# Optimization experiments

Measured on AMD Instinct MI355X. Metric: run time of the kernel, lower is better.

## Reference

```python
import jax, jax.numpy as jnp
import numpy as np

B, T, I, H = 4096, 512, 3, 64


def setup_inputs() -> dict:
    key = jax.random.key(0)
    ks = jax.random.split(key, 8)
    s = 1.0 / np.sqrt(H)  # PyTorch LSTM init scale
    x = jax.random.normal(ks[0], (B, T, I), dtype=jnp.float32)
    W_ih = jax.random.uniform(ks[1], (4 * H, I), minval=-s, maxval=s, dtype=jnp.float32)
    W_hh = jax.random.uniform(ks[2], (4 * H, H), minval=-s, maxval=s, dtype=jnp.float32)
    b_ih = jax.random.uniform(ks[3], (4 * H,), minval=-s, maxval=s, dtype=jnp.float32)
    b_hh = jax.random.uniform(ks[4], (4 * H,), minval=-s, maxval=s, dtype=jnp.float32)
    W_dec = jax.random.uniform(ks[5], (I, H), minval=-s, maxval=s, dtype=jnp.float32)
    b_dec = jax.random.uniform(ks[6], (I,), minval=-s, maxval=s, dtype=jnp.float32)
    return {"x": x, "W_ih": W_ih, "W_hh": W_hh, "b_ih": b_ih, "b_hh": b_hh,
            "W_dec": W_dec, "b_dec": b_dec}


def _lstm(x, W_ih, W_hh, b_ih, b_hh):
    # Precompute input contribution for all timesteps: [B, T, 4H]
    x_gates = jnp.einsum('bti,gi->btg', x, W_ih) + b_ih + b_hh
    h0 = jnp.zeros((x.shape[0], H), dtype=x.dtype)
    c0 = jnp.zeros((x.shape[0], H), dtype=x.dtype)

    def step(carry, xg_t):
        h, c = carry
        gates = xg_t + h @ W_hh.T  # [B, 4H]
        i_g, f_g, g_g, o_g = jnp.split(gates, 4, axis=-1)  # PyTorch order i,f,g,o
        i_g = jax.nn.sigmoid(i_g)
        f_g = jax.nn.sigmoid(f_g)
        g_g = jnp.tanh(g_g)
        o_g = jax.nn.sigmoid(o_g)
        c_new = f_g * c + i_g * g_g
        h_new = o_g * jnp.tanh(c_new)
        return (h_new, c_new), h_new

    _, hs = jax.lax.scan(step, (h0, c0), jnp.swapaxes(x_gates, 0, 1))  # [T, B, H]
    return jnp.swapaxes(hs, 0, 1)  # [B, T, H]


def reference(x, W_ih, W_hh, b_ih, b_hh, W_dec, b_dec):
    lstm_out = _lstm(x, W_ih, W_hh, b_ih, b_hh)
    return jnp.einsum('bth,oh->bto', lstm_out, W_dec) + b_dec  # [B, T, I]
```

## Files before the change

kernel.cpp:

```cpp
#include <hip/hip_runtime.h>


#define TLEN 512
#define TCHUNK 64
#define ROWS 16

typedef float    float4_t __attribute__((ext_vector_type(4)));
typedef _Float16 halfx8   __attribute__((ext_vector_type(8)));

#define INV2048 4.8828125e-4f

__device__ __forceinline__ float fexp2(float x){ return __builtin_amdgcn_exp2f(x); }
__device__ __forceinline__ float frcp (float x){ return __builtin_amdgcn_rcpf(x); }
__device__ __forceinline__ float sigm (float x){ return frcp(1.f + fexp2(-1.44269504f*x)); }
__device__ __forceinline__ float tanh_(float x){ return 1.f - 2.f*frcp(1.f + fexp2(2.88539008f*x)); }

__device__ __forceinline__ unsigned short hbits(_Float16 h){
  union { _Float16 h; unsigned short u; } x; x.h = h; return x.u;
}

__device__ __forceinline__ void split8h(const float* v, halfx8& hi, halfx8& lo){
  #pragma unroll
  for (int j = 0; j < 8; j++){
    _Float16 h = (_Float16)v[j];
    hi[j] = h;
    lo[j] = (_Float16)((v[j] - (float)h) * 2048.0f);
  }
}

#define MFMA(a,b,c) __builtin_amdgcn_mfma_f32_16x16x32_f16((a),(b),(c),0,0,0)

#define HHI 0
#define HS_SZ 2304
#define XOF 0
#define XPK 3136
#define OOF0 7232
#define OOF1 10368
#define LF_SZ 13504

__global__ __launch_bounds__(320, 1)
void LSTMAnomalyDetector_kernel(
    const float* __restrict__ x,     const float* __restrict__ W_ih,
    const float* __restrict__ W_hh,  const float* __restrict__ b_ih,
    const float* __restrict__ b_hh,  const float* __restrict__ W_dec,
    const float* __restrict__ b_dec, float* __restrict__ out)
{
  __shared__ __align__(16) unsigned short HS[HS_SZ];
  __shared__ __align__(16) float          LF[LF_SZ];

  const int tid  = threadIdx.x;
  const int w    = tid >> 6;
  const int lane = tid & 63;
  const int q    = lane >> 4;
  const int lid  = lane & 15;
  const int b0   = blockIdx.x * ROWS;
  const int cw   = (w & 3)*16 + lid;

  halfx8 Bh[4][2], Bl[4][2];
  halfx8 Dh[2];
  float  wi[4][3], bsum[4];

  if (w < 4){
    #pragma unroll
    for (int tl = 0; tl < 4; tl++){
      const int g = tl*64 + cw;
      #pragma unroll
      for (int kt = 0; kt < 2; kt++){
        const float* p = W_hh + g*64 + kt*32 + q*8;
        float v[8];
        #pragma unroll
        for (int j = 0; j < 8; j++) v[j] = p[j];
        split8h(v, Bh[tl][kt], Bl[tl][kt]);
      }
      wi[tl][0] = W_ih[g*3+0];
      wi[tl][1] = W_ih[g*3+1];
      wi[tl][2] = W_ih[g*3+2];
      bsum[tl]  = b_ih[g] + b_hh[g];
    }
  } else {
    #pragma unroll
    for (int kt = 0; kt < 2; kt++){
      #pragma unroll
      for (int j = 0; j < 8; j++) Dh[kt][j] = (_Float16)0.f;
      if (lid < 3){
        const float* p = W_dec + lid*64 + kt*32 + q*8;
        #pragma unroll
        for (int j = 0; j < 8; j++) Dh[kt][j] = (_Float16)p[j];
      }
    }
  }
  const float bdec = (lid < 3) ? b_dec[lid] : 0.f;

  halfx8 ah0 = {}, ah1 = {};
  float creg[4] = {0.f, 0.f, 0.f, 0.f};
  float4_t xp4[4];

  auto loadx = [&](int d){
    #pragma unroll
    for (int r = 0; r < 4; r++){
      float4_t xv = *(const float4_t*)&LF[XPK + d*64 + (q*4+r)*4];
      #pragma unroll
      for (int tl = 0; tl < 4; tl++)
        xp4[tl][r] = fmaf(wi[tl][2], xv[2],
                      fmaf(wi[tl][1], xv[1],
                        fmaf(wi[tl][0], xv[0], bsum[tl])));
    }
  };

  if (w < 4){
    #pragma unroll
    for (int s = 0; s < 3; s++){
      const int f = tid + 256*s;
      const int row = f/48; const int off = (f%48)*4;
      float4_t v = *(const float4_t*)(x + (size_t)(b0+row)*1536 + off);
      *(float4_t*)&LF[XOF + row*196 + off] = v;
    }
  }
  __syncthreads();
  if (w < 4){
    #pragma unroll
    for (int s = 0; s < 4; s++){
      const int p = tid + 256*s;
      const float* xr = &LF[XOF + (p & 15)*196 + (p >> 4)*3];
      float4_t v = {xr[0], xr[1], xr[2], 0.f};
      *(float4_t*)&LF[XPK + p*4] = v;
    }
  }
  __syncthreads();
  if (w < 4) loadx(0);

  for (int t = 0; t < TLEN; ++t){
    const int dt = t & (TCHUNK-1);
    const int hb = (t & 1) * 1152;

    if (w < 4){
      float4_t c1 = xp4[3];
      c1 = MFMA(ah0, Bh[3][0], c1);
      c1 = MFMA(ah1, Bh[3][1], c1);
      float4_t c2 = {0.f,0.f,0.f,0.f};
      c2 = MFMA(ah0, Bl[3][0], c2);
      c2 = MFMA(ah1, Bl[3][1], c2);
      float4_t og;
      #pragma unroll
      for (int r = 0; r < 4; r++) og[r] = sigm(fmaf(c2[r], INV2048, c1[r]));

      c1 = xp4[1];
      c1 = MFMA(ah0, Bh[1][0], c1);
      c1 = MFMA(ah1, Bh[1][1], c1);
      c2 = (float4_t){0.f,0.f,0.f,0.f};
      c2 = MFMA(ah0, Bl[1][0], c2);
      c2 = MFMA(ah1, Bl[1][1], c2);
      float4_t cp;
      #pragma unroll
      for (int r = 0; r < 4; r++){
        const float fg = sigm(fmaf(c2[r], INV2048, c1[r]));
        cp[r] = fg * creg[r];
      }

      c1 = xp4[0];
      c1 = MFMA(ah0, Bh[0][0], c1);
      c1 = MFMA(ah1, Bh[0][1], c1);
      c2 = (float4_t){0.f,0.f,0.f,0.f};
      c2 = MFMA(ah0, Bl[0][0], c2);
      c2 = MFMA(ah1, Bl[0][1], c2);
      float4_t ig;
      #pragma unroll
      for (int r = 0; r < 4; r++) ig[r] = sigm(fmaf(c2[r], INV2048, c1[r]));

      c1 = xp4[2];
      c1 = MFMA(ah0, Bh[2][0], c1);
      c1 = MFMA(ah1, Bh[2][1], c1);
      c2 = (float4_t){0.f,0.f,0.f,0.f};
      c2 = MFMA(ah0, Bl[2][0], c2);
      c2 = MFMA(ah1, Bl[2][1], c2);
      #pragma unroll
      for (int r = 0; r < 4; r++){
        const float gg = tanh_(fmaf(c2[r], INV2048, c1[r]));
        creg[r] = fmaf(ig[r], gg, cp[r]);
        const float h = og[r] * tanh_(creg[r]);
        const _Float16 h16 = (_Float16)h;
        HS[HHI + hb + (q*4+r)*72 + cw] = hbits(h16);
      }

      if (dt != TCHUNK-1) loadx(dt+1);
    } else {
      if (t > 0){
        const int hbp = (1 - (t & 1)) * 1152;
        const unsigned short* ph = &HS[HHI + hbp + lid*72 + q*8];
        halfx8 dh0 = *(const halfx8*)&ph[0];
        halfx8 dh1 = *(const halfx8*)&ph[32];
        float4_t d1 = {0.f,0.f,0.f,0.f};
        d1 = MFMA(dh0, Dh[0], d1);
        d1 = MFMA(dh1, Dh[1], d1);
        if (lid < 3){
          const int tp  = t - 1;
          const int oof = OOF0 + ((tp >> 6) & 1) * 3136;
          const int dto = tp & (TCHUNK-1);
          #pragma unroll
          for (int r = 0; r < 4; r++)
            LF[oof + (q*4+r)*196 + dto*3 + lid] = d1[r] + bdec;
        }
      }
    }

    __syncthreads();

    if (w < 4){
      const unsigned short* ph = &HS[HHI + hb + lid*72 + q*8];
      ah0 = *(const halfx8*)&ph[0];
      ah1 = *(const halfx8*)&ph[32];

      if (dt == 1 && t > TCHUNK){
        const int ckf = (t >> 6) - 1;
        const int oof = OOF0 + (ckf & 1) * 3136;
        const int t0  = ckf * TCHUNK;
        #pragma unroll
        for (int s = 0; s < 3; s++){
          const int f = tid + 256*s;
          const int row = f/48; const int off = (f%48)*4;
          float4_t v = *(const float4_t*)&LF[oof + row*196 + off];
          *(float4_t*)(out + (size_t)(b0+row)*1536 + t0*3 + off) = v;
        }
      }
    }

    if (dt == TCHUNK-1){
      if (t + 1 < TLEN){
        if (w < 4){
          #pragma unroll
          for (int s = 0; s < 3; s++){
            const int f = tid + 256*s;
            const int row = f/48; const int off = (f%48)*4;
            float4_t v = *(const float4_t*)(x + (size_t)(b0+row)*1536 + (t+1)*3 + off);
            *(float4_t*)&LF[XOF + row*196 + off] = v;
          }
        }
        __syncthreads();
        if (w < 4){
          #pragma unroll
          for (int s = 0; s < 4; s++){
            const int p = tid + 256*s;
            const float* xr = &LF[XOF + (p & 15)*196 + (p >> 4)*3];
            float4_t v = {xr[0], xr[1], xr[2], 0.f};
            *(float4_t*)&LF[XPK + p*4] = v;
          }
        }
      }
      __syncthreads();
      if (w < 4 && t + 1 < TLEN) loadx(0);
    }
  }

  if (w == 4){
    const int hbp = ((TLEN-1) & 1) * 1152;
    const unsigned short* ph = &HS[HHI + hbp + lid*72 + q*8];
    halfx8 dh0 = *(const halfx8*)&ph[0];
    halfx8 dh1 = *(const halfx8*)&ph[32];
    float4_t d1 = {0.f,0.f,0.f,0.f};
    d1 = MFMA(dh0, Dh[0], d1);
    d1 = MFMA(dh1, Dh[1], d1);
    if (lid < 3){
      const int oof = OOF0 + (((TLEN-1) >> 6) & 1) * 3136;
      #pragma unroll
      for (int r = 0; r < 4; r++)
        LF[oof + (q*4+r)*196 + 63*3 + lid] = d1[r] + bdec;
    }
  }
  __syncthreads();
  if (w < 4){
    const int ckf = (TLEN >> 6) - 1;
    const int oof = OOF0 + (ckf & 1) * 3136;
    const int t0  = ckf * TCHUNK;
    #pragma unroll
    for (int s = 0; s < 3; s++){
      const int f = tid + 256*s;
      const int row = f/48; const int off = (f%48)*4;
      float4_t v = *(const float4_t*)&LF[oof + row*196 + off];
      *(float4_t*)(out + (size_t)(b0+row)*1536 + t0*3 + off) = v;
    }
  }
}

extern "C" void kernel_launch(void* const* d_in, const int* in_sizes, int n_in,
                              void* d_out, int out_size, void* d_ws, size_t ws_size,
                              hipStream_t stream)
{
  const float* x     = (const float*)d_in[0];
  const float* W_ih  = (const float*)d_in[1];
  const float* W_hh  = (const float*)d_in[2];
  const float* b_ih  = (const float*)d_in[3];
  const float* b_hh  = (const float*)d_in[4];
  const float* W_dec = (const float*)d_in[5];
  const float* b_dec = (const float*)d_in[6];
  float* out = (float*)d_out;

  const int B = in_sizes[0] / (TLEN * 3);
  const int blocks = B / ROWS;
  hipLaunchKernelGGL(LSTMAnomalyDetector_kernel, dim3(blocks), dim3(320), 0, stream,
                     x, W_ih, W_hh, b_ih, b_hh, W_dec, b_dec, out);
}
```

Baseline: 426.0 us.

## Halve rows per block and redistribute duplicated MFMA rows across quads via shuffles

Each block now handles 8 batch rows instead of 16, so there are twice as many blocks, and launch bounds allow two blocks per CU. The 16-row MFMA tile now carries duplicated rows. Each lane swaps gate pre-activations with its partner 32 lanes away, so every lane evaluates transcendentals for only 2 unique rows instead of 4, which halves per-lane activation work. The cost is that MFMA throughput is wasted on duplicate rows, cross-lane shuffles are added, and two resident blocks must share the CU's matrix units and LDS.

```diff
diff --git a/kernel.cpp b/kernel.cpp
--- a/kernel.cpp
+++ b/kernel.cpp
@@ -3,7 +3,7 @@
 
 #define TLEN 512
 #define TCHUNK 64
-#define ROWS 16
+#define ROWS 8
 
 typedef float    float4_t __attribute__((ext_vector_type(4)));
 typedef _Float16 halfx8   __attribute__((ext_vector_type(8)));
@@ -33,12 +33,12 @@
 #define HHI 0
 #define HS_SZ 2304
 #define XOF 0
-#define XPK 3136
-#define OOF0 7232
-#define OOF1 10368
-#define LF_SZ 13504
-
-__global__ __launch_bounds__(320, 1)
+#define XPK 1568
+#define OOF0 3616
+#define OOF1 5184
+#define LF_SZ 6752
+
+__global__ __launch_bounds__(320, 2)
 void LSTMAnomalyDetector_kernel(
     const float* __restrict__ x,     const float* __restrict__ W_ih,
     const float* __restrict__ W_hh,  const float* __restrict__ b_ih,
@@ -55,6 +55,8 @@
   const int lid  = lane & 15;
   const int b0   = blockIdx.x * ROWS;
   const int cw   = (w & 3)*16 + lid;
+  const bool hiq = (q < 2);
+  const int  row0 = (q & 1)*4 + (q >> 1)*2;
 
   halfx8 Bh[4][2], Bl[4][2];
   halfx8 Dh[2];
@@ -92,13 +94,14 @@
   const float bdec = (lid < 3) ? b_dec[lid] : 0.f;
 
   halfx8 ah0 = {}, ah1 = {};
-  float creg[4] = {0.f, 0.f, 0.f, 0.f};
+  float creg[2] = {0.f, 0.f};
   float4_t xp4[4];
 
   auto loadx = [&](int d){
     #pragma unroll
     for (int r = 0; r < 4; r++){
-      float4_t xv = *(const float4_t*)&LF[XPK + d*64 + (q*4+r)*4];
+      const int rr = (q*4 + r) & 7;
+      float4_t xv = *(const float4_t*)&LF[XPK + d*32 + rr*4];
       #pragma unroll
       for (int tl = 0; tl < 4; tl++)
         xp4[tl][r] = fmaf(wi[tl][2], xv[2],
@@ -109,19 +112,21 @@
 
   if (w < 4){
     #pragma unroll
-    for (int s = 0; s < 3; s++){
+    for (int s = 0; s < 2; s++){
       const int f = tid + 256*s;
-      const int row = f/48; const int off = (f%48)*4;
-      float4_t v = *(const float4_t*)(x + (size_t)(b0+row)*1536 + off);
-      *(float4_t*)&LF[XOF + row*196 + off] = v;
+      if (f < 384){
+        const int row = f/48; const int off = (f%48)*4;
+        float4_t v = *(const float4_t*)(x + (size_t)(b0+row)*1536 + off);
+        *(float4_t*)&LF[XOF + row*196 + off] = v;
+      }
     }
   }
   __syncthreads();
   if (w < 4){
     #pragma unroll
-    for (int s = 0; s < 4; s++){
+    for (int s = 0; s < 2; s++){
       const int p = tid + 256*s;
-      const float* xr = &LF[XOF + (p & 15)*196 + (p >> 4)*3];
+      const float* xr = &LF[XOF + (p & 7)*196 + (p >> 3)*3];
       float4_t v = {xr[0], xr[1], xr[2], 0.f};
       *(float4_t*)&LF[XPK + p*4] = v;
     }
@@ -140,9 +145,13 @@
       float4_t c2 = {0.f,0.f,0.f,0.f};
       c2 = MFMA(ah0, Bl[3][0], c2);
       c2 = MFMA(ah1, Bl[3][1], c2);
-      float4_t og;
-      #pragma unroll
-      for (int r = 0; r < 4; r++) og[r] = sigm(fmaf(c2[r], INV2048, c1[r]));
+      float4_t to;
+      #pragma unroll
+      for (int r = 0; r < 4; r++) to[r] = fmaf(c2[r], INV2048, c1[r]);
+      const float ro2 = __shfl_xor(to[2], 32, 64);
+      const float ro3 = __shfl_xor(to[3], 32, 64);
+      const float og0 = sigm(hiq ? to[0] : ro2);
+      const float og1 = sigm(hiq ? to[1] : ro3);
 
       c1 = xp4[1];
       c1 = MFMA(ah0, Bh[1][0], c1);
@@ -150,12 +159,13 @@
       c2 = (float4_t){0.f,0.f,0.f,0.f};
       c2 = MFMA(ah0, Bl[1][0], c2);
       c2 = MFMA(ah1, Bl[1][1], c2);
-      float4_t cp;
-      #pragma unroll
-      for (int r = 0; r < 4; r++){
-        const float fg = sigm(fmaf(c2[r], INV2048, c1[r]));
-        cp[r] = fg * creg[r];
-      }
+      float4_t tf;
+      #pragma unroll
+      for (int r = 0; r < 4; r++) tf[r] = fmaf(c2[r], INV2048, c1[r]);
+      const float rf2 = __shfl_xor(tf[2], 32, 64);
+      const float rf3 = __shfl_xor(tf[3], 32, 64);
+      const float cp0 = sigm(hiq ? tf[0] : rf2) * creg[0];
+      const float cp1 = sigm(hiq ? tf[1] : rf3) * creg[1];
 
       c1 = xp4[0];
       c1 = MFMA(ah0, Bh[0][0], c1);
@@ -163,9 +173,13 @@
       c2 = (float4_t){0.f,0.f,0.f,0.f};
       c2 = MFMA(ah0, Bl[0][0], c2);
       c2 = MFMA(ah1, Bl[0][1], c2);
-      float4_t ig;
-      #pragma unroll
-      for (int r = 0; r < 4; r++) ig[r] = sigm(fmaf(c2[r], INV2048, c1[r]));
+      float4_t ti;
+      #pragma unroll
+      for (int r = 0; r < 4; r++) ti[r] = fmaf(c2[r], INV2048, c1[r]);
+      const float ri2 = __shfl_xor(ti[2], 32, 64);
+      const float ri3 = __shfl_xor(ti[3], 32, 64);
+      const float ig0 = sigm(hiq ? ti[0] : ri2);
+      const float ig1 = sigm(hiq ? ti[1] : ri3);
 
       c1 = xp4[2];
       c1 = MFMA(ah0, Bh[2][0], c1);
@@ -173,13 +187,22 @@
       c2 = (float4_t){0.f,0.f,0.f,0.f};
       c2 = MFMA(ah0, Bl[2][0], c2);
       c2 = MFMA(ah1, Bl[2][1], c2);
-      #pragma unroll
-      for (int r = 0; r < 4; r++){
-        const float gg = tanh_(fmaf(c2[r], INV2048, c1[r]));
-        creg[r] = fmaf(ig[r], gg, cp[r]);
-        const float h = og[r] * tanh_(creg[r]);
-        const _Float16 h16 = (_Float16)h;
-        HS[HHI + hb + (q*4+r)*72 + cw] = hbits(h16);
+      float4_t tg;
+      #pragma unroll
+      for (int r = 0; r < 4; r++) tg[r] = fmaf(c2[r], INV2048, c1[r]);
+      const float rg2 = __shfl_xor(tg[2], 32, 64);
+      const float rg3 = __shfl_xor(tg[3], 32, 64);
+      {
+        const float gg = tanh_(hiq ? tg[0] : rg2);
+        creg[0] = fmaf(ig0, gg, cp0);
+        const float h = og0 * tanh_(creg[0]);
+        HS[HHI + hb + row0*72 + cw] = hbits((_Float16)h);
+      }
+      {
+        const float gg = tanh_(hiq ? tg[1] : rg3);
+        creg[1] = fmaf(ig1, gg, cp1);
+        const float h = og1 * tanh_(creg[1]);
+        HS[HHI + hb + (row0+1)*72 + cw] = hbits((_Float16)h);
       }
 
       if (dt != TCHUNK-1) loadx(dt+1);
@@ -192,9 +215,9 @@
         float4_t d1 = {0.f,0.f,0.f,0.f};
         d1 = MFMA(dh0, Dh[0], d1);
         d1 = MFMA(dh1, Dh[1], d1);
-        if (lid < 3){
+        if (lid < 3 && q < 2){
           const int tp  = t - 1;
-          const int oof = OOF0 + ((tp >> 6) & 1) * 3136;
+          const int oof = OOF0 + ((tp >> 6) & 1) * 1568;
           const int dto = tp & (TCHUNK-1);
           #pragma unroll
           for (int r = 0; r < 4; r++)
@@ -212,14 +235,16 @@
 
       if (dt == 1 && t > TCHUNK){
         const int ckf = (t >> 6) - 1;
-        const int oof = OOF0 + (ckf & 1) * 3136;
+        const int oof = OOF0 + (ckf & 1) * 1568;
         const int t0  = ckf * TCHUNK;
         #pragma unroll
-        for (int s = 0; s < 3; s++){
+        for (int s = 0; s < 2; s++){
           const int f = tid + 256*s;
-          const int row = f/48; const int off = (f%48)*4;
-          float4_t v = *(const float4_t*)&LF[oof + row*196 + off];
-          *(float4_t*)(out + (size_t)(b0+row)*1536 + t0*3 + off) = v;
+          if (f < 384){
+            const int row = f/48; const int off = (f%48)*4;
+            float4_t v = *(const float4_t*)&LF[oof + row*196 + off];
+            *(float4_t*)(out + (size_t)(b0+row)*1536 + t0*3 + off) = v;
+          }
         }
       }
     }
@@ -228,19 +253,21 @@
       if (t + 1 < TLEN){
         if (w < 4){
           #pragma unroll
-          for (int s = 0; s < 3; s++){
+          for (int s = 0; s < 2; s++){
             const int f = tid + 256*s;
-            const int row = f/48; const int off = (f%48)*4;
-            float4_t v = *(const float4_t*)(x + (size_t)(b0+row)*1536 + (t+1)*3 + off);
-            *(float4_t*)&LF[XOF + row*196 + off] = v;
+            if (f < 384){
+              const int row = f/48; const int off = (f%48)*4;
+              float4_t v = *(const float4_t*)(x + (size_t)(b0+row)*1536 + (t+1)*3 + off);
+              *(float4_t*)&LF[XOF + row*196 + off] = v;
+            }
           }
         }
         __syncthreads();
         if (w < 4){
           #pragma unroll
-          for (int s = 0; s < 4; s++){
+          for (int s = 0; s < 2; s++){
             const int p = tid + 256*s;
-            const float* xr = &LF[XOF + (p & 15)*196 + (p >> 4)*3];
+            const float* xr = &LF[XOF + (p & 7)*196 + (p >> 3)*3];
             float4_t v = {xr[0], xr[1], xr[2], 0.f};
             *(float4_t*)&LF[XPK + p*4] = v;
           }
@@ -259,8 +286,8 @@
     float4_t d1 = {0.f,0.f,0.f,0.f};
     d1 = MFMA(dh0, Dh[0], d1);
     d1 = MFMA(dh1, Dh[1], d1);
-    if (lid < 3){
-      const int oof = OOF0 + (((TLEN-1) >> 6) & 1) * 3136;
+    if (lid < 3 && q < 2){
+      const int oof = OOF0 + (((TLEN-1) >> 6) & 1) * 1568;
       #pragma unroll
       for (int r = 0; r < 4; r++)
         LF[oof + (q*4+r)*196 + 63*3 + lid] = d1[r] + bdec;
@@ -269,14 +296,16 @@
   __syncthreads();
   if (w < 4){
     const int ckf = (TLEN >> 6) - 1;
-    const int oof = OOF0 + (ckf & 1) * 3136;
+    const int oof = OOF0 + (ckf & 1) * 1568;
     const int t0  = ckf * TCHUNK;
     #pragma unroll
-    for (int s = 0; s < 3; s++){
+    for (int s = 0; s < 2; s++){
       const int f = tid + 256*s;
-      const int row = f/48; const int off = (f%48)*4;
-      float4_t v = *(const float4_t*)&LF[oof + row*196 + off];
-      *(float4_t*)(out + (size_t)(b0+row)*1536 + t0*3 + off) = v;
+      if (f < 384){
+        const int row = f/48; const int off = (f%48)*4;
+        float4_t v = *(const float4_t*)&LF[oof + row*196 + off];
+        *(float4_t*)(out + (size_t)(b0+row)*1536 + t0*3 + off) = v;
+      }
     }
   }
 }
```

New measurement: 791.2 us. 1.86x slower.
